# Optimization experiments

Hardware: AMD Instinct MI355X
Metric: run time of the kernel (lower is better)

The kernel has to match this reference:

```python
import jax, jax.numpy as jnp
import numpy as np

B, D, K = 32768, 1024, 64
N3, N4, N5 = 512, 512, 512


def setup_inputs() -> dict:
    key = jax.random.key(0)
    ks = jax.random.split(key, 10)
    # x in [-1, 1]^D as the docstring states
    x = jax.random.uniform(ks[0], (B, D), dtype=jnp.float32, minval=-1.0, maxval=1.0)
    S = jnp.sort(jax.random.randint(ks[1], (K,), 0, D, dtype=jnp.int32))
    a = jax.random.normal(ks[2], (K,), dtype=jnp.float32)
    b = jax.random.normal(ks[3], (K, K), dtype=jnp.float32)
    idx3 = jax.random.randint(ks[4], (N3, 3), 0, K, dtype=jnp.int32)
    c3 = jax.random.normal(ks[5], (N3,), dtype=jnp.float32)
    idx4 = jax.random.randint(ks[6], (N4, 4), 0, K, dtype=jnp.int32)
    c4 = jax.random.normal(ks[7], (N4,), dtype=jnp.float32)
    idx5 = jax.random.randint(ks[8], (N5, 5), 0, K, dtype=jnp.int32)
    c5 = jax.random.normal(ks[9], (N5,), dtype=jnp.float32)
    return {"x": x, "S": S, "a": a, "b": b, "idx3": idx3, "c3": c3,
            "idx4": idx4, "c4": c4, "idx5": idx5, "c5": c5}


def _monomial_term(xS, idx, c):
    # xS: (B,k); idx: (n,deg); c: (n,) -> (B,)
    # gather -> (B, n, deg), product over monomial factors, weighted sum
    prod = jnp.prod(xS[:, idx], axis=2)  # (B, n)
    return prod @ c


def reference(x, S, a, b, idx3, c3, idx4, c4, idx5, c5):
    xS = x[:, S]                      # (B, k)
    lin = xS @ a                      # (B,)
    # sum_{i<j} b[i,j] xS_i xS_j == einsum with strictly-upper-triangular b
    bu = jnp.triu(b, k=1)             # (k, k)
    quad = jnp.einsum('bi,ij,bj->b', xS, bu, xS)
    out = lin + quad
    out = out + _monomial_term(xS, idx3, c3)
    out = out + _monomial_term(xS, idx4, c4)
    out = out + _monomial_term(xS, idx5, c5)
    return out
```

## Files before the change

### kernel.cpp

```cpp
#include <hip/hip_runtime.h>
#include <hip/hip_fp16.h>
#include <stdint.h>

#define NT 256
#define RPB 32
#define XSTR 80

#define WS_P3   0
#define WS_P4   4096
#define WS_P5   12288
#define WS_BUTH 20480

static __device__ __forceinline__ __half2 H2(unsigned u) {
    return __builtin_bit_cast(__half2, u);
}
static __device__ __forceinline__ unsigned short f2hbits(float f) {
    __half h = __float2half(f);
    return __builtin_bit_cast(unsigned short, h);
}

__global__ void prepack(const float* __restrict__ b,
                        const int* __restrict__ i3, const float* __restrict__ c3,
                        const int* __restrict__ i4, const float* __restrict__ c4,
                        const int* __restrict__ i5, const float* __restrict__ c5,
                        unsigned char* __restrict__ ws)
{
    const int g = blockIdx.x * NT + threadIdx.x;
    if (g < 4096) {
        int j = g >> 6, i = g & 63;
        float v = (i < j) ? b[i * 64 + j] : 0.0f;
        ((unsigned short*)(ws + WS_BUTH))[g] = f2hbits(v);
    }
    if (g < 512) {
        unsigned o0, o1, o2, o3, o4;
        o0 = (unsigned)i3[3*g+0] * XSTR; o1 = (unsigned)i3[3*g+1] * XSTR; o2 = (unsigned)i3[3*g+2] * XSTR;
        ((uint2*)(ws + WS_P3))[g] = make_uint2(o0 | (o1 << 16), o2 | ((unsigned)f2hbits(c3[g]) << 16));
        o0 = (unsigned)i4[4*g+0] * XSTR; o1 = (unsigned)i4[4*g+1] * XSTR;
        o2 = (unsigned)i4[4*g+2] * XSTR; o3 = (unsigned)i4[4*g+3] * XSTR;
        ((uint4*)(ws + WS_P4))[g] = make_uint4(o0 | (o1 << 16), o2 | (o3 << 16), (unsigned)f2hbits(c4[g]), 0u);
        o0 = (unsigned)i5[5*g+0] * XSTR; o1 = (unsigned)i5[5*g+1] * XSTR;
        o2 = (unsigned)i5[5*g+2] * XSTR; o3 = (unsigned)i5[5*g+3] * XSTR;
        o4 = (unsigned)i5[5*g+4] * XSTR;
        ((uint4*)(ws + WS_P5))[g] = make_uint4(o0 | (o1 << 16), o2 | (o3 << 16), o4 | ((unsigned)f2hbits(c5[g]) << 16), 0u);
    }
}

static __device__ __forceinline__ void qfma(__half2 bb, uint4 xk, __half2 d[4]) {
    d[0] = __hfma2(bb, H2(xk.x), d[0]);
    d[1] = __hfma2(bb, H2(xk.y), d[1]);
    d[2] = __hfma2(bb, H2(xk.z), d[2]);
    d[3] = __hfma2(bb, H2(xk.w), d[3]);
}
static __device__ __forceinline__ void pmul(const uint4& a, __half2 p[4]) {
    p[0] = __hmul2(p[0], H2(a.x));
    p[1] = __hmul2(p[1], H2(a.y));
    p[2] = __hmul2(p[2], H2(a.z));
    p[3] = __hmul2(p[3], H2(a.w));
}
static __device__ __forceinline__ void pacc(__half2 c2, const __half2 p[4], __half2 acc[4]) {
    acc[0] = __hfma2(c2, p[0], acc[0]);
    acc[1] = __hfma2(c2, p[1], acc[1]);
    acc[2] = __hfma2(c2, p[2], acc[2]);
    acc[3] = __hfma2(c2, p[3], acc[3]);
}

__global__ __launch_bounds__(NT, 4)
void poly_main(const float* __restrict__ x, const int* __restrict__ S,
               const float* __restrict__ a,
               const unsigned char* __restrict__ ws, float* __restrict__ out)
{
    __shared__ __align__(16) __half xS[64 * 40];
    __shared__ float red[4][4][8];

    const int tid  = threadIdx.x;
    const int row0 = blockIdx.x * RPB;

    {
        const int k = tid & 63, q = tid >> 6;
        const int sk = S[k];
        const float* xc = x + (size_t)row0 * 1024 + sk;
        float v[8];
        #pragma unroll
        for (int m = 0; m < 8; ++m) v[m] = xc[(size_t)(q * 8 + m) * 1024];
        uint4 pk;
        pk.x = __builtin_bit_cast(unsigned, __floats2half2_rn(v[0], v[1]));
        pk.y = __builtin_bit_cast(unsigned, __floats2half2_rn(v[2], v[3]));
        pk.z = __builtin_bit_cast(unsigned, __floats2half2_rn(v[4], v[5]));
        pk.w = __builtin_bit_cast(unsigned, __floats2half2_rn(v[6], v[7]));
        *(uint4*)((char*)xS + k * XSTR + q * 16) = pk;
    }
    __syncthreads();

    const int rg = tid & 3;
    const int ts = tid >> 2;
    const char* xb = (const char*)xS + rg * 16;

    __half2 d[4] = {H2(0u), H2(0u), H2(0u), H2(0u)};
    {
        const uint4* buTh4 = (const uint4*)(ws + WS_BUTH) + ts * 8;
        const int nii = (ts + 7) >> 3;
        #pragma unroll 2
        for (int g = 0; g < nii; ++g) {
            uint4 bw = buTh4[g];
            const char* xkb = xb + g * 8 * XSTR;
            unsigned pw[4] = {bw.x, bw.y, bw.z, bw.w};
            #pragma unroll
            for (int p = 0; p < 4; ++p) {
                __half2 blo = __half2half2(__ushort_as_half((unsigned short)(pw[p] & 0xFFFFu)));
                __half2 bhi = __half2half2(__ushort_as_half((unsigned short)(pw[p] >> 16)));
                uint4 x0 = *(const uint4*)(xkb + (2 * p + 0) * XSTR);
                uint4 x1 = *(const uint4*)(xkb + (2 * p + 1) * XSTR);
                qfma(blo, x0, d);
                qfma(bhi, x1, d);
            }
        }
    }
    __half2 acc[4];
    {
        __half2 a2 = __half2half2(__float2half(a[ts]));
        uint4 xj = *(const uint4*)(xb + ts * XSTR);
        acc[0] = __hmul2(__hadd2(a2, d[0]), H2(xj.x));
        acc[1] = __hmul2(__hadd2(a2, d[1]), H2(xj.y));
        acc[2] = __hmul2(__hadd2(a2, d[2]), H2(xj.z));
        acc[3] = __hmul2(__hadd2(a2, d[3]), H2(xj.w));
    }

    const uint2* p3 = (const uint2*)(ws + WS_P3);
    const uint4* p4 = (const uint4*)(ws + WS_P4);
    const uint4* p5 = (const uint4*)(ws + WS_P5);

    #pragma unroll 4
    for (int m = 0; m < 8; ++m) {
        uint2 p = p3[64 * m + ts];
        uint4 v0 = *(const uint4*)(xb + (p.x & 0xFFFFu));
        uint4 v1 = *(const uint4*)(xb + (p.x >> 16));
        uint4 v2 = *(const uint4*)(xb + (p.y & 0xFFFFu));
        __half2 pr[4] = {H2(v0.x), H2(v0.y), H2(v0.z), H2(v0.w)};
        pmul(v1, pr);
        pmul(v2, pr);
        pacc(__half2half2(__ushort_as_half((unsigned short)(p.y >> 16))), pr, acc);
    }
    #pragma unroll 2
    for (int m = 0; m < 8; ++m) {
        uint4 p = p4[64 * m + ts];
        uint4 v0 = *(const uint4*)(xb + (p.x & 0xFFFFu));
        uint4 v1 = *(const uint4*)(xb + (p.x >> 16));
        uint4 v2 = *(const uint4*)(xb + (p.y & 0xFFFFu));
        uint4 v3 = *(const uint4*)(xb + (p.y >> 16));
        __half2 pr[4] = {H2(v0.x), H2(v0.y), H2(v0.z), H2(v0.w)};
        pmul(v1, pr);
        pmul(v2, pr);
        pmul(v3, pr);
        pacc(__half2half2(__ushort_as_half((unsigned short)(p.z & 0xFFFFu))), pr, acc);
    }
    #pragma unroll 2
    for (int m = 0; m < 8; ++m) {
        uint4 p = p5[64 * m + ts];
        uint4 v0 = *(const uint4*)(xb + (p.x & 0xFFFFu));
        uint4 v1 = *(const uint4*)(xb + (p.x >> 16));
        uint4 v2 = *(const uint4*)(xb + (p.y & 0xFFFFu));
        uint4 v3 = *(const uint4*)(xb + (p.y >> 16));
        uint4 v4 = *(const uint4*)(xb + (p.z & 0xFFFFu));
        __half2 pr[4] = {H2(v0.x), H2(v0.y), H2(v0.z), H2(v0.w)};
        pmul(v1, pr);
        pmul(v2, pr);
        pmul(v3, pr);
        pmul(v4, pr);
        pacc(__half2half2(__ushort_as_half((unsigned short)(p.z >> 16))), pr, acc);
    }

    float f[8];
    #pragma unroll
    for (int e = 0; e < 4; ++e) {
        f[2 * e]     = __low2float(acc[e]);
        f[2 * e + 1] = __high2float(acc[e]);
    }
    #pragma unroll
    for (int mask = 4; mask <= 32; mask <<= 1) {
        #pragma unroll
        for (int r = 0; r < 8; ++r) f[r] += __shfl_xor(f[r], mask, 64);
    }
    const int w = tid >> 6, lane = tid & 63;
    if (lane < 4) {
        #pragma unroll
        for (int r = 0; r < 8; ++r) red[w][lane][r] = f[r];
    }
    __syncthreads();
    if (tid < 32) {
        int g = tid >> 3, e = tid & 7;
        out[row0 + tid] = red[0][g][e] + red[1][g][e] + red[2][g][e] + red[3][g][e];
    }
}

extern "C" void kernel_launch(void* const* d_in, const int* in_sizes, int n_in,
                              void* d_out, int out_size, void* d_ws, size_t ws_size,
                              hipStream_t stream) {
    const float* x  = (const float*)d_in[0];
    const int*   S  = (const int*)d_in[1];
    const float* a  = (const float*)d_in[2];
    const float* b  = (const float*)d_in[3];
    const int*   i3 = (const int*)d_in[4];
    const float* c3 = (const float*)d_in[5];
    const int*   i4 = (const int*)d_in[6];
    const float* c4 = (const float*)d_in[7];
    const int*   i5 = (const int*)d_in[8];
    const float* c5 = (const float*)d_in[9];
    unsigned char* ws = (unsigned char*)d_ws;
    float* out = (float*)d_out;

    prepack<<<16, NT, 0, stream>>>(b, i3, c3, i4, c4, i5, c5, ws);
    poly_main<<<32768 / RPB, NT, 0, stream>>>(x, S, a, ws, out);
}
```

Before: 210.1 us.

## Prefetch per-thread monomial tables into registers before the x gather

The prepack kernel now lays out the monomial descriptor tables so each thread's eight entries are contiguous. The main kernel loads all of them, plus the triangular b row and a[ts], into registers with wide vector loads issued before the strided x gather and barrier. This hides their latency behind the gather and removes dependent global loads from the compute loops, which are now fully unrolled. The cost is many more live registers (around 100 VGPRs for the prefetched data), which may hurt occupancy under launch_bounds(256,4) or cause spills.

```diff
diff --git a/kernel.cpp b/kernel.cpp
--- a/kernel.cpp
+++ b/kernel.cpp
@@ -32,16 +32,17 @@
         ((unsigned short*)(ws + WS_BUTH))[g] = f2hbits(v);
     }
     if (g < 512) {
+        const int slot = (g & 63) * 8 + (g >> 6);
         unsigned o0, o1, o2, o3, o4;
         o0 = (unsigned)i3[3*g+0] * XSTR; o1 = (unsigned)i3[3*g+1] * XSTR; o2 = (unsigned)i3[3*g+2] * XSTR;
-        ((uint2*)(ws + WS_P3))[g] = make_uint2(o0 | (o1 << 16), o2 | ((unsigned)f2hbits(c3[g]) << 16));
+        ((uint2*)(ws + WS_P3))[slot] = make_uint2(o0 | (o1 << 16), o2 | ((unsigned)f2hbits(c3[g]) << 16));
         o0 = (unsigned)i4[4*g+0] * XSTR; o1 = (unsigned)i4[4*g+1] * XSTR;
         o2 = (unsigned)i4[4*g+2] * XSTR; o3 = (unsigned)i4[4*g+3] * XSTR;
-        ((uint4*)(ws + WS_P4))[g] = make_uint4(o0 | (o1 << 16), o2 | (o3 << 16), (unsigned)f2hbits(c4[g]), 0u);
+        ((uint4*)(ws + WS_P4))[slot] = make_uint4(o0 | (o1 << 16), o2 | (o3 << 16), (unsigned)f2hbits(c4[g]), 0u);
         o0 = (unsigned)i5[5*g+0] * XSTR; o1 = (unsigned)i5[5*g+1] * XSTR;
         o2 = (unsigned)i5[5*g+2] * XSTR; o3 = (unsigned)i5[5*g+3] * XSTR;
         o4 = (unsigned)i5[5*g+4] * XSTR;
-        ((uint4*)(ws + WS_P5))[g] = make_uint4(o0 | (o1 << 16), o2 | (o3 << 16), o4 | ((unsigned)f2hbits(c5[g]) << 16), 0u);
+        ((uint4*)(ws + WS_P5))[slot] = make_uint4(o0 | (o1 << 16), o2 | (o3 << 16), o4 | ((unsigned)f2hbits(c5[g]) << 16), 0u);
     }
 }
 
@@ -75,6 +76,27 @@
     const int tid  = threadIdx.x;
     const int row0 = blockIdx.x * RPB;
 
+    const int rg = tid & 3;
+    const int ts = tid >> 2;
+
+    uint2 e3[8];
+    uint4 e4[8], e5[8], bw[8];
+    {
+        const uint4* s3 = (const uint4*)(ws + WS_P3 + ts * 64);
+        #pragma unroll
+        for (int i = 0; i < 4; ++i) ((uint4*)e3)[i] = s3[i];
+        const uint4* s4 = (const uint4*)(ws + WS_P4 + ts * 128);
+        #pragma unroll
+        for (int i = 0; i < 8; ++i) e4[i] = s4[i];
+        const uint4* s5 = (const uint4*)(ws + WS_P5 + ts * 128);
+        #pragma unroll
+        for (int i = 0; i < 8; ++i) e5[i] = s5[i];
+        const uint4* sb = (const uint4*)(ws + WS_BUTH + ts * 128);
+        #pragma unroll
+        for (int i = 0; i < 8; ++i) bw[i] = sb[i];
+    }
+    const float av = a[ts];
+
     {
         const int k = tid & 63, q = tid >> 6;
         const int sk = S[k];
@@ -91,33 +113,32 @@
     }
     __syncthreads();
 
-    const int rg = tid & 3;
-    const int ts = tid >> 2;
     const char* xb = (const char*)xS + rg * 16;
 
     __half2 d[4] = {H2(0u), H2(0u), H2(0u), H2(0u)};
     {
-        const uint4* buTh4 = (const uint4*)(ws + WS_BUTH) + ts * 8;
         const int nii = (ts + 7) >> 3;
-        #pragma unroll 2
-        for (int g = 0; g < nii; ++g) {
-            uint4 bw = buTh4[g];
-            const char* xkb = xb + g * 8 * XSTR;
-            unsigned pw[4] = {bw.x, bw.y, bw.z, bw.w};
-            #pragma unroll
-            for (int p = 0; p < 4; ++p) {
-                __half2 blo = __half2half2(__ushort_as_half((unsigned short)(pw[p] & 0xFFFFu)));
-                __half2 bhi = __half2half2(__ushort_as_half((unsigned short)(pw[p] >> 16)));
-                uint4 x0 = *(const uint4*)(xkb + (2 * p + 0) * XSTR);
-                uint4 x1 = *(const uint4*)(xkb + (2 * p + 1) * XSTR);
-                qfma(blo, x0, d);
-                qfma(bhi, x1, d);
+        #pragma unroll
+        for (int g = 0; g < 8; ++g) {
+            if (g < nii) {
+                uint4 w4 = bw[g];
+                const char* xkb = xb + g * 8 * XSTR;
+                unsigned pw[4] = {w4.x, w4.y, w4.z, w4.w};
+                #pragma unroll
+                for (int p = 0; p < 4; ++p) {
+                    __half2 blo = __half2half2(__ushort_as_half((unsigned short)(pw[p] & 0xFFFFu)));
+                    __half2 bhi = __half2half2(__ushort_as_half((unsigned short)(pw[p] >> 16)));
+                    uint4 x0 = *(const uint4*)(xkb + (2 * p + 0) * XSTR);
+                    uint4 x1 = *(const uint4*)(xkb + (2 * p + 1) * XSTR);
+                    qfma(blo, x0, d);
+                    qfma(bhi, x1, d);
+                }
             }
         }
     }
     __half2 acc[4];
     {
-        __half2 a2 = __half2half2(__float2half(a[ts]));
+        __half2 a2 = __half2half2(__float2half(av));
         uint4 xj = *(const uint4*)(xb + ts * XSTR);
         acc[0] = __hmul2(__hadd2(a2, d[0]), H2(xj.x));
         acc[1] = __hmul2(__hadd2(a2, d[1]), H2(xj.y));
@@ -125,13 +146,9 @@
         acc[3] = __hmul2(__hadd2(a2, d[3]), H2(xj.w));
     }
 
-    const uint2* p3 = (const uint2*)(ws + WS_P3);
-    const uint4* p4 = (const uint4*)(ws + WS_P4);
-    const uint4* p5 = (const uint4*)(ws + WS_P5);
-
-    #pragma unroll 4
+    #pragma unroll
     for (int m = 0; m < 8; ++m) {
-        uint2 p = p3[64 * m + ts];
+        uint2 p = e3[m];
         uint4 v0 = *(const uint4*)(xb + (p.x & 0xFFFFu));
         uint4 v1 = *(const uint4*)(xb + (p.x >> 16));
         uint4 v2 = *(const uint4*)(xb + (p.y & 0xFFFFu));
@@ -140,9 +157,9 @@
         pmul(v2, pr);
         pacc(__half2half2(__ushort_as_half((unsigned short)(p.y >> 16))), pr, acc);
     }
-    #pragma unroll 2
+    #pragma unroll
     for (int m = 0; m < 8; ++m) {
-        uint4 p = p4[64 * m + ts];
+        uint4 p = e4[m];
         uint4 v0 = *(const uint4*)(xb + (p.x & 0xFFFFu));
         uint4 v1 = *(const uint4*)(xb + (p.x >> 16));
         uint4 v2 = *(const uint4*)(xb + (p.y & 0xFFFFu));
@@ -153,9 +170,9 @@
         pmul(v3, pr);
         pacc(__half2half2(__ushort_as_half((unsigned short)(p.z & 0xFFFFu))), pr, acc);
     }
-    #pragma unroll 2
+    #pragma unroll
     for (int m = 0; m < 8; ++m) {
-        uint4 p = p5[64 * m + ts];
+        uint4 p = e5[m];
         uint4 v0 = *(const uint4*)(xb + (p.x & 0xFFFFu));
         uint4 v1 = *(const uint4*)(xb + (p.x >> 16));
         uint4 v2 = *(const uint4*)(xb + (p.y & 0xFFFFu));
```

Result: faster. 204.9 us (-2.5%).
